# Kernel tuning notes

Measured on AMD Instinct MI355X. Metric: run time of the kernel, lower is better.

The kernel has to match this reference:

```python
import jax, jax.numpy as jnp
import numpy as np

S, B, D = 2048, 64, 1024  # seq_len, batch, 2*hidden_size


def setup_inputs() -> dict:
    key = jax.random.key(0)
    k1, k2, k3 = jax.random.split(key, 3)
    hidden = jax.random.normal(k1, (1, B, D), dtype=jnp.float32)
    encoder_outputs = jax.random.normal(k2, (S, B, D), dtype=jnp.float32)
    W_attn = jax.random.normal(k3, (D, D), dtype=jnp.float32) * (1.0 / np.sqrt(D))
    b_attn = jnp.zeros((D,), dtype=jnp.float32)
    return {"hidden": hidden, "encoder_outputs": encoder_outputs,
            "W_attn": W_attn, "b_attn": b_attn}


def reference(hidden, encoder_outputs, W_attn, b_attn):
    # method='general': energy[b,i] = hidden[0,b] . (W @ enc[i,b] + bias)
    # nn.Linear computes x @ W.T + b -> einsum over last dim with W rows as outputs
    proj = jnp.einsum('sbd,ed->sbe', encoder_outputs, W_attn) + b_attn  # [S,B,D]
    energies = jnp.einsum('bd,sbd->bs', hidden[0], proj)                # [B,S]
    return jax.nn.softmax(energies, axis=1)[:, None, :]                 # [B,1,S]
```

## Files before the change

### kernel.cpp

```cpp
#include <hip/hip_runtime.h>
#include <math.h>

#define SS 2048
#define BB 64
#define DD 1024

__global__ __launch_bounds__(256) void proj_vec_kernel(
    const float* __restrict__ h, const float* __restrict__ W, float* __restrict__ v) {
    int dl = threadIdx.x & 63;
    int eg = threadIdx.x >> 6;
    int d  = blockIdx.x * 64 + dl;
    int b0 = blockIdx.y * 4;
    int e0 = eg * 256;
    const float* h0 = h + (size_t)(b0 + 0) * DD + e0;
    const float* h1 = h + (size_t)(b0 + 1) * DD + e0;
    const float* h2 = h + (size_t)(b0 + 2) * DD + e0;
    const float* h3 = h + (size_t)(b0 + 3) * DD + e0;
    const float* Wp = W + (size_t)e0 * DD + d;
    float a0 = 0.f, a1 = 0.f, a2 = 0.f, a3 = 0.f;
    #pragma unroll 8
    for (int e = 0; e < 256; ++e) {
        float w = Wp[(size_t)e * DD];
        a0 = fmaf(h0[e], w, a0);
        a1 = fmaf(h1[e], w, a1);
        a2 = fmaf(h2[e], w, a2);
        a3 = fmaf(h3[e], w, a3);
    }
    __shared__ float red[4][4][64];
    red[eg][0][dl] = a0; red[eg][1][dl] = a1;
    red[eg][2][dl] = a2; red[eg][3][dl] = a3;
    __syncthreads();
    if (eg == 0) {
        #pragma unroll
        for (int j = 0; j < 4; ++j) {
            float s = red[0][j][dl] + red[1][j][dl] + red[2][j][dl] + red[3][j][dl];
            v[(size_t)(b0 + j) * DD + d] = s;
        }
    }
}

__global__ __launch_bounds__(256) void energy_kernel(
    const float* __restrict__ enc, const float* __restrict__ vv, float* __restrict__ e_out) {
    int wid  = (blockIdx.x * 256 + threadIdx.x) >> 6;
    int lane = threadIdx.x & 63;
    int b  = wid & (BB - 1);
    int sc = wid >> 6;
    const float4* vr = (const float4*)(vv + (size_t)b * DD);
    float4 w0 = vr[lane];
    float4 w1 = vr[lane + 64];
    float4 w2 = vr[lane + 128];
    float4 w3 = vr[lane + 192];
    int s0 = sc * 16;
    #pragma unroll 1
    for (int i = 0; i < 16; i += 2) {
        const float4* r0 = (const float4*)(enc + ((size_t)(s0 + i)     * BB + b) * DD);
        const float4* r1 = (const float4*)(enc + ((size_t)(s0 + i + 1) * BB + b) * DD);
        float4 a0 = r0[lane];
        float4 a1 = r0[lane + 64];
        float4 a2 = r0[lane + 128];
        float4 a3 = r0[lane + 192];
        float4 c0 = r1[lane];
        float4 c1 = r1[lane + 64];
        float4 c2 = r1[lane + 128];
        float4 c3 = r1[lane + 192];
        float p = a0.x*w0.x + a0.y*w0.y + a0.z*w0.z + a0.w*w0.w
                + a1.x*w1.x + a1.y*w1.y + a1.z*w1.z + a1.w*w1.w
                + a2.x*w2.x + a2.y*w2.y + a2.z*w2.z + a2.w*w2.w
                + a3.x*w3.x + a3.y*w3.y + a3.z*w3.z + a3.w*w3.w;
        float q = c0.x*w0.x + c0.y*w0.y + c0.z*w0.z + c0.w*w0.w
                + c1.x*w1.x + c1.y*w1.y + c1.z*w1.z + c1.w*w1.w
                + c2.x*w2.x + c2.y*w2.y + c2.z*w2.z + c2.w*w2.w
                + c3.x*w3.x + c3.y*w3.y + c3.z*w3.z + c3.w*w3.w;
        #pragma unroll
        for (int off = 32; off; off >>= 1) {
            p += __shfl_xor(p, off, 64);
            q += __shfl_xor(q, off, 64);
        }
        if (lane == 0) {
            e_out[b * SS + s0 + i]     = p;
            e_out[b * SS + s0 + i + 1] = q;
        }
    }
}

__global__ __launch_bounds__(256) void softmax_kernel(
    const float* __restrict__ e_in, float* __restrict__ out) {
    int b   = blockIdx.x;
    int tid = threadIdx.x;
    __shared__ float red[256];
    float vals[8];
    float m = -INFINITY;
    #pragma unroll
    for (int k = 0; k < 8; ++k) {
        vals[k] = e_in[b * SS + tid + 256 * k];
        m = fmaxf(m, vals[k]);
    }
    red[tid] = m;
    __syncthreads();
    for (int off = 128; off > 0; off >>= 1) {
        if (tid < off) red[tid] = fmaxf(red[tid], red[tid + off]);
        __syncthreads();
    }
    m = red[0];
    __syncthreads();
    float sum = 0.f;
    #pragma unroll
    for (int k = 0; k < 8; ++k) {
        vals[k] = expf(vals[k] - m);
        sum += vals[k];
    }
    red[tid] = sum;
    __syncthreads();
    for (int off = 128; off > 0; off >>= 1) {
        if (tid < off) red[tid] += red[tid + off];
        __syncthreads();
    }
    float inv = 1.0f / red[0];
    #pragma unroll
    for (int k = 0; k < 8; ++k)
        out[b * SS + tid + 256 * k] = vals[k] * inv;
}

extern "C" void kernel_launch(void* const* d_in, const int* in_sizes, int n_in,
                              void* d_out, int out_size, void* d_ws, size_t ws_size,
                              hipStream_t stream) {
    const float* hidden = (const float*)d_in[0];
    const float* enc    = (const float*)d_in[1];
    const float* W      = (const float*)d_in[2];
    float* out = (float*)d_out;

    float* v    = (float*)d_ws;
    float* e_ws = (float*)((char*)d_ws + BB * DD * sizeof(float));

    dim3 gA(DD / 64, BB / 4);
    proj_vec_kernel<<<gA, 256, 0, stream>>>(hidden, W, v);
    energy_kernel<<<2048, 256, 0, stream>>>(enc, v, e_ws);
    softmax_kernel<<<BB, 256, 0, stream>>>(e_ws, out);
}
```

Before: 129.6 us.

## Split projection reduction across 8 wave groups and batch energy reductions through LDS

The projection kernel now uses 512 threads, so each of 8 wave groups covers 128 of the e dimension, and four waves share the final reduction. In the energy kernel each wave stores its 16 per-lane partial dot products to shared memory and reduces them together afterwards. This replaces 16 six-step shuffle reductions per wave with a short LDS sum plus two shuffles. The cost is an added block barrier and 16KB of shared memory per block. The enc loads are also now issued one row at a time with an unroll of 2, instead of two rows per iteration.

```diff
diff --git a/kernel.cpp b/kernel.cpp
--- a/kernel.cpp
+++ b/kernel.cpp
@@ -5,13 +5,13 @@
 #define BB 64
 #define DD 1024
 
-__global__ __launch_bounds__(256) void proj_vec_kernel(
+__global__ __launch_bounds__(512) void proj_vec_kernel(
     const float* __restrict__ h, const float* __restrict__ W, float* __restrict__ v) {
     int dl = threadIdx.x & 63;
     int eg = threadIdx.x >> 6;
     int d  = blockIdx.x * 64 + dl;
     int b0 = blockIdx.y * 4;
-    int e0 = eg * 256;
+    int e0 = eg * 128;
     const float* h0 = h + (size_t)(b0 + 0) * DD + e0;
     const float* h1 = h + (size_t)(b0 + 1) * DD + e0;
     const float* h2 = h + (size_t)(b0 + 2) * DD + e0;
@@ -19,30 +19,32 @@
     const float* Wp = W + (size_t)e0 * DD + d;
     float a0 = 0.f, a1 = 0.f, a2 = 0.f, a3 = 0.f;
     #pragma unroll 8
-    for (int e = 0; e < 256; ++e) {
+    for (int e = 0; e < 128; ++e) {
         float w = Wp[(size_t)e * DD];
         a0 = fmaf(h0[e], w, a0);
         a1 = fmaf(h1[e], w, a1);
         a2 = fmaf(h2[e], w, a2);
         a3 = fmaf(h3[e], w, a3);
     }
-    __shared__ float red[4][4][64];
+    __shared__ float red[8][4][64];
     red[eg][0][dl] = a0; red[eg][1][dl] = a1;
     red[eg][2][dl] = a2; red[eg][3][dl] = a3;
     __syncthreads();
-    if (eg == 0) {
+    if (eg < 4) {
+        float s = 0.f;
         #pragma unroll
-        for (int j = 0; j < 4; ++j) {
-            float s = red[0][j][dl] + red[1][j][dl] + red[2][j][dl] + red[3][j][dl];
-            v[(size_t)(b0 + j) * DD + d] = s;
-        }
+        for (int g = 0; g < 8; ++g) s += red[g][eg][dl];
+        v[(size_t)(b0 + eg) * DD + d] = s;
     }
 }
 
 __global__ __launch_bounds__(256) void energy_kernel(
     const float* __restrict__ enc, const float* __restrict__ vv, float* __restrict__ e_out) {
-    int wid  = (blockIdx.x * 256 + threadIdx.x) >> 6;
-    int lane = threadIdx.x & 63;
+    __shared__ float part[4][16][65];
+    int tid  = threadIdx.x;
+    int w    = tid >> 6;
+    int lane = tid & 63;
+    int wid  = blockIdx.x * 4 + w;
     int b  = wid & (BB - 1);
     int sc = wid >> 6;
     const float4* vr = (const float4*)(vv + (size_t)b * DD);
@@ -51,36 +53,28 @@
     float4 w2 = vr[lane + 128];
     float4 w3 = vr[lane + 192];
     int s0 = sc * 16;
-    #pragma unroll 1
-    for (int i = 0; i < 16; i += 2) {
-        const float4* r0 = (const float4*)(enc + ((size_t)(s0 + i)     * BB + b) * DD);
-        const float4* r1 = (const float4*)(enc + ((size_t)(s0 + i + 1) * BB + b) * DD);
+    #pragma unroll 2
+    for (int i = 0; i < 16; ++i) {
+        const float4* r0 = (const float4*)(enc + ((size_t)(s0 + i) * BB + b) * DD);
         float4 a0 = r0[lane];
         float4 a1 = r0[lane + 64];
         float4 a2 = r0[lane + 128];
         float4 a3 = r0[lane + 192];
-        float4 c0 = r1[lane];
-        float4 c1 = r1[lane + 64];
-        float4 c2 = r1[lane + 128];
-        float4 c3 = r1[lane + 192];
         float p = a0.x*w0.x + a0.y*w0.y + a0.z*w0.z + a0.w*w0.w
                 + a1.x*w1.x + a1.y*w1.y + a1.z*w1.z + a1.w*w1.w
                 + a2.x*w2.x + a2.y*w2.y + a2.z*w2.z + a2.w*w2.w
                 + a3.x*w3.x + a3.y*w3.y + a3.z*w3.z + a3.w*w3.w;
-        float q = c0.x*w0.x + c0.y*w0.y + c0.z*w0.z + c0.w*w0.w
-                + c1.x*w1.x + c1.y*w1.y + c1.z*w1.z + c1.w*w1.w
-                + c2.x*w2.x + c2.y*w2.y + c2.z*w2.z + c2.w*w2.w
-                + c3.x*w3.x + c3.y*w3.y + c3.z*w3.z + c3.w*w3.w;
-        #pragma unroll
-        for (int off = 32; off; off >>= 1) {
-            p += __shfl_xor(p, off, 64);
-            q += __shfl_xor(q, off, 64);
-        }
-        if (lane == 0) {
-            e_out[b * SS + s0 + i]     = p;
-            e_out[b * SS + s0 + i + 1] = q;
-        }
+        part[w][i][lane] = p;
     }
+    __syncthreads();
+    int r  = lane >> 2;
+    int qd = lane & 3;
+    float sum = 0.f;
+    #pragma unroll
+    for (int k = 0; k < 16; ++k) sum += part[w][r][qd * 16 + k];
+    sum += __shfl_xor(sum, 1, 64);
+    sum += __shfl_xor(sum, 2, 64);
+    if (qd == 0) e_out[b * SS + s0 + r] = sum;
 }
 
 __global__ __launch_bounds__(256) void softmax_kernel(
@@ -133,7 +127,7 @@
     float* e_ws = (float*)((char*)d_ws + BB * DD * sizeof(float));
 
     dim3 gA(DD / 64, BB / 4);
-    proj_vec_kernel<<<gA, 256, 0, stream>>>(hidden, W, v);
+    proj_vec_kernel<<<gA, 512, 0, stream>>>(hidden, W, v);
     energy_kernel<<<2048, 256, 0, stream>>>(enc, v, e_ws);
     softmax_kernel<<<BB, 256, 0, stream>>>(e_ws, out);
 }
```

Result: faster. 114.5 us (-11.7%).
